# Optimization experiments

Hardware: AMD Instinct MI355X
Metric: run time of the kernel (lower is better)

The kernel has to match this reference:

```python
import jax, jax.numpy as jnp
import numpy as np

B, N, D, L = 8, 2048, 64, 3

def setup_inputs() -> dict:
    key = jax.random.key(0)
    ks = jax.random.split(key, 8)
    x = jax.random.normal(ks[0], (B, N, D), dtype=jnp.float32)
    # binary adjacency with self-loops so every node degree >= 1
    adj = (jax.random.uniform(ks[1], (B, N, N)) < 0.01).astype(jnp.float32)
    adj = jnp.maximum(adj, jnp.eye(N, dtype=jnp.float32)[None])
    # xavier-style params
    U0 = jax.random.normal(ks[2], (D, D), dtype=jnp.float32) * np.sqrt(2.0 / (D + D))
    b0 = jax.random.uniform(ks[3], (D,), dtype=jnp.float32)
    Us = jax.random.normal(ks[4], (L, D, D), dtype=jnp.float32) * np.sqrt(2.0 / (D + D))
    Q = jax.random.normal(ks[5], (D, D), dtype=jnp.float32) * np.sqrt(2.0 / (D + D))
    P = jax.random.normal(ks[6], (1, D), dtype=jnp.float32) * np.sqrt(2.0 / (1 + D))
    return {"x": x, "adj_mat": adj, "U0": U0, "b0": b0, "Us": Us, "Q": Q, "P": P}

def reference(x, adj_mat, U0, b0, Us, Q, P):
    h = x @ U0 + b0  # [B,N,D]
    mask = (adj_mat > 0).astype(h.dtype)          # [B,N,N]
    deg = adj_mat.sum(axis=1)                      # [B,N] (column sums, matches torch sum(axis=1))
    for l in range(Us.shape[0]):
        agg = jnp.einsum('bji,bjd->bid', mask, h)  # masked neighbor sum per node i
        h = jax.nn.relu((agg @ Us[l]) / deg[..., None])
    m = h.sum(axis=1) / h.shape[1]                 # [B,D] mean over nodes
    out = (P @ jax.nn.relu(Q @ m.T)).squeeze()     # [B]
    return out
```

## Files before the change

### kernel.cpp

```cpp
#include <hip/hip_runtime.h>

#define B 8
#define N 2048
#define D 64
#define BN (B*N)
#define CAP 64

__global__ __launch_bounds__(256) void kSLP(
        const float* __restrict__ adj, const float* __restrict__ x,
        const float* __restrict__ U0, const float* __restrict__ b0,
        unsigned short* __restrict__ cols, int* __restrict__ cnt,
        float* __restrict__ h0) {
    __shared__ unsigned sh[64 * 65 + 64];
    const int tid = threadIdx.x;
    const int bid = blockIdx.x;
    if (bid < 256) {
        unsigned (*lmask)[65] = (unsigned(*)[65])sh;
        int b  = bid >> 5, ck = bid & 31;
        int jb = tid >> 5;
        int cp = tid & 31;
        int c0 = cp * 2, c1 = cp * 2 + 1;
        const float* base = adj + (size_t)b * N * N + (size_t)(jb * 256) * N
                            + ck * 64 + cp * 2;
        for (int ws = 0; ws < 8; ++ws) {
            unsigned w0 = 0, w1 = 0;
#pragma unroll 8
            for (int i = 0; i < 32; ++i) {
                float2 v = *(const float2*)(base + (size_t)(ws * 32 + i) * N);
                w0 |= (v.x != 0.f ? 1u : 0u) << i;
                w1 |= (v.y != 0.f ? 1u : 0u) << i;
            }
            lmask[c0][jb * 8 + ws] = w0;
            lmask[c1][jb * 8 + ws] = w1;
        }
        __syncthreads();
        if (tid < 64) {
            int gcol = b * N + ck * 64 + tid;
            unsigned short* cl = cols + (size_t)gcol * CAP;
            int p = 0;
            for (int w = 0; w < 64; ++w) {
                unsigned m = lmask[tid][w];
                int jbase = w * 32;
                while (m) {
                    int t = __builtin_ctz(m);
                    m &= m - 1;
                    if (p < CAP) cl[p] = (unsigned short)(jbase + t);
                    ++p;
                }
            }
            cnt[gcol] = p;
        }
    } else {
        float* Uld = (float*)sh;
        float* bld = (float*)sh + 4096;
#pragma unroll
        for (int q = 0; q < 16; ++q) Uld[tid + q * 256] = U0[tid + q * 256];
        if (tid < D) bld[tid] = b0[tid];
        __syncthreads();
        int wid = tid >> 6, lane = tid & 63;
        int gw = (bid - 256) * 4 + wid;
        for (int rr = 0; rr < 16; ++rr) {
            int r = gw * 16 + rr;
            float xv = x[(size_t)r * D + lane];
            float o0 = bld[lane], o1 = 0.f, o2 = 0.f, o3 = 0.f;
#pragma unroll
            for (int k = 0; k < D; k += 4) {
                o0 = fmaf(__shfl(xv, k),     Uld[(k)     * D + lane], o0);
                o1 = fmaf(__shfl(xv, k + 1), Uld[(k + 1) * D + lane], o1);
                o2 = fmaf(__shfl(xv, k + 2), Uld[(k + 2) * D + lane], o2);
                o3 = fmaf(__shfl(xv, k + 3), Uld[(k + 3) * D + lane], o3);
            }
            h0[(size_t)r * D + lane] = (o0 + o1) + (o2 + o3);
        }
    }
}

__global__ __launch_bounds__(256) void kL(const float* __restrict__ hin,
        const unsigned short* __restrict__ cols, const int* __restrict__ cnt,
        const float* __restrict__ U, float* __restrict__ hout,
        float* __restrict__ pg) {
    __shared__ float Uld[D * D];
    __shared__ float part[4][D];
    const int tid = threadIdx.x;
    const int bid = blockIdx.x;
#pragma unroll
    for (int q = 0; q < 16; ++q) Uld[tid + q * 256] = U[tid + q * 256];
    __syncthreads();
    int wid = tid >> 6, lane = tid & 63;
    int r0 = bid * 8 + wid * 2, r1 = r0 + 1;
    const float* hb = hin + ((size_t)(r0 >> 11) << 11) * D;
    int ca = cnt[r0], cb = cnt[r1];
    int kma = ca < CAP ? ca : CAP, kmb = cb < CAP ? cb : CAP;
    const unsigned short* la = cols + (size_t)r0 * CAP;
    const unsigned short* lb = cols + (size_t)r1 * CAP;
    float acca = 0.f, accb = 0.f;
    int km = kma > kmb ? kma : kmb;
    for (int k = 0; k < km; k += 8) {
        uint4 wa = *(const uint4*)(la + k);
        uint4 wb = *(const uint4*)(lb + k);
        float a0 = hb[(size_t)(wa.x & 0xffff) * D + lane];
        float a1 = hb[(size_t)(wa.x >> 16)    * D + lane];
        float a2 = hb[(size_t)(wa.y & 0xffff) * D + lane];
        float a3 = hb[(size_t)(wa.y >> 16)    * D + lane];
        float a4 = hb[(size_t)(wa.z & 0xffff) * D + lane];
        float a5 = hb[(size_t)(wa.z >> 16)    * D + lane];
        float a6 = hb[(size_t)(wa.w & 0xffff) * D + lane];
        float a7 = hb[(size_t)(wa.w >> 16)    * D + lane];
        float b0_ = hb[(size_t)(wb.x & 0xffff) * D + lane];
        float b1_ = hb[(size_t)(wb.x >> 16)    * D + lane];
        float b2_ = hb[(size_t)(wb.y & 0xffff) * D + lane];
        float b3_ = hb[(size_t)(wb.y >> 16)    * D + lane];
        float b4_ = hb[(size_t)(wb.z & 0xffff) * D + lane];
        float b5_ = hb[(size_t)(wb.z >> 16)    * D + lane];
        float b6_ = hb[(size_t)(wb.w & 0xffff) * D + lane];
        float b7_ = hb[(size_t)(wb.w >> 16)    * D + lane];
        acca += ((k + 0 < kma ? a0 : 0.f) + (k + 1 < kma ? a1 : 0.f))
              + ((k + 2 < kma ? a2 : 0.f) + (k + 3 < kma ? a3 : 0.f))
              + ((k + 4 < kma ? a4 : 0.f) + (k + 5 < kma ? a5 : 0.f))
              + ((k + 6 < kma ? a6 : 0.f) + (k + 7 < kma ? a7 : 0.f));
        accb += ((k + 0 < kmb ? b0_ : 0.f) + (k + 1 < kmb ? b1_ : 0.f))
              + ((k + 2 < kmb ? b2_ : 0.f) + (k + 3 < kmb ? b3_ : 0.f))
              + ((k + 4 < kmb ? b4_ : 0.f) + (k + 5 < kmb ? b5_ : 0.f))
              + ((k + 6 < kmb ? b6_ : 0.f) + (k + 7 < kmb ? b7_ : 0.f));
    }
    float oa0 = 0.f, oa1 = 0.f, oa2 = 0.f, oa3 = 0.f;
    float ob0 = 0.f, ob1 = 0.f, ob2 = 0.f, ob3 = 0.f;
#pragma unroll
    for (int d = 0; d < D; d += 4) {
        oa0 = fmaf(__shfl(acca, d),     Uld[(d)     * D + lane], oa0);
        ob0 = fmaf(__shfl(accb, d),     Uld[(d)     * D + lane], ob0);
        oa1 = fmaf(__shfl(acca, d + 1), Uld[(d + 1) * D + lane], oa1);
        ob1 = fmaf(__shfl(accb, d + 1), Uld[(d + 1) * D + lane], ob1);
        oa2 = fmaf(__shfl(acca, d + 2), Uld[(d + 2) * D + lane], oa2);
        ob2 = fmaf(__shfl(accb, d + 2), Uld[(d + 2) * D + lane], ob2);
        oa3 = fmaf(__shfl(acca, d + 3), Uld[(d + 3) * D + lane], oa3);
        ob3 = fmaf(__shfl(accb, d + 3), Uld[(d + 3) * D + lane], ob3);
    }
    float outa = fmaxf(((oa0 + oa1) + (oa2 + oa3)) / (float)ca, 0.f);
    float outb = fmaxf(((ob0 + ob1) + (ob2 + ob3)) / (float)cb, 0.f);
    hout[(size_t)r0 * D + lane] = outa;
    hout[(size_t)r1 * D + lane] = outb;
    if (pg != nullptr) {
        part[wid][lane] = outa + outb;
        __syncthreads();
        if (wid == 0)
            pg[(size_t)bid * D + lane] =
                part[0][lane] + part[1][lane] + part[2][lane] + part[3][lane];
    }
}

__global__ __launch_bounds__(512) void kHead(const float* __restrict__ pg,
        const float* __restrict__ Q, const float* __restrict__ P,
        float* __restrict__ out) {
    int wid = threadIdx.x >> 6, lane = threadIdx.x & 63;
    float md = 0.f;
#pragma unroll 8
    for (int k = 0; k < 256; ++k) md += pg[(size_t)(wid * 256 + k) * D + lane];
    md *= (1.0f / N);
    float t = 0.f;
#pragma unroll 8
    for (int k = 0; k < D; ++k) t = fmaf(Q[lane * D + k], __shfl(md, k), t);
    t = fmaxf(t, 0.f);
    float v = t * P[lane];
    for (int off = 32; off; off >>= 1) v += __shfl_down(v, off);
    if (lane == 0) out[wid] = v;
}

extern "C" void kernel_launch(void* const* d_in, const int* in_sizes, int n_in,
                              void* d_out, int out_size, void* d_ws, size_t ws_size,
                              hipStream_t stream) {
    const float* x   = (const float*)d_in[0];
    const float* adj = (const float*)d_in[1];
    const float* U0  = (const float*)d_in[2];
    const float* b0  = (const float*)d_in[3];
    const float* Us  = (const float*)d_in[4];
    const float* Q   = (const float*)d_in[5];
    const float* P   = (const float*)d_in[6];
    float* out = (float*)d_out;

    char* ws = (char*)d_ws;
    size_t off = 0;
    float* h0 = (float*)(ws + off); off += (size_t)BN * D * sizeof(float);
    float* h1 = (float*)(ws + off); off += (size_t)BN * D * sizeof(float);
    unsigned short* cols = (unsigned short*)(ws + off);
    off += (size_t)CAP * BN * sizeof(unsigned short);
    int* cnt = (int*)(ws + off); off += (size_t)BN * sizeof(int);
    float* pg = (float*)(ws + off); off += (size_t)2048 * D * sizeof(float);

    kSLP<<<512, 256, 0, stream>>>(adj, x, U0, b0, cols, cnt, h0);
    kL<<<2048, 256, 0, stream>>>(h0, cols, cnt, Us + 0 * D * D, h1, nullptr);
    kL<<<2048, 256, 0, stream>>>(h1, cols, cnt, Us + 1 * D * D, h0, nullptr);
    kL<<<2048, 256, 0, stream>>>(h0, cols, cnt, Us + 2 * D * D, h1, pg);
    kHead<<<1, 512, 0, stream>>>(pg, Q, P, out);
}
```

Before: 109.2 us.

## Widen adjacency scan to 1024-thread blocks with float4 loads, prefetch neighbor indices

The adjacency-to-list scan now uses 1024-thread blocks where each thread reads a 32-row strip of four columns with float4 loads, replacing the eight sequential strips per thread. The aim is more memory requests in flight for the dominant 128 MB adjacency read. The projection half is remapped to fit the larger block. The layer kernel software-prefetches the next group of neighbor indices and masks them to 11 bits, since the prefetch may read past a node's list.

```diff
diff --git a/kernel.cpp b/kernel.cpp
--- a/kernel.cpp
+++ b/kernel.cpp
@@ -6,7 +6,7 @@
 #define BN (B*N)
 #define CAP 64
 
-__global__ __launch_bounds__(256) void kSLP(
+__global__ __launch_bounds__(1024, 8) void kScanProj(
         const float* __restrict__ adj, const float* __restrict__ x,
         const float* __restrict__ U0, const float* __restrict__ b0,
         unsigned short* __restrict__ cols, int* __restrict__ cnt,
@@ -17,22 +17,23 @@
     if (bid < 256) {
         unsigned (*lmask)[65] = (unsigned(*)[65])sh;
         int b  = bid >> 5, ck = bid & 31;
-        int jb = tid >> 5;
-        int cp = tid & 31;
-        int c0 = cp * 2, c1 = cp * 2 + 1;
-        const float* base = adj + (size_t)b * N * N + (size_t)(jb * 256) * N
-                            + ck * 64 + cp * 2;
-        for (int ws = 0; ws < 8; ++ws) {
-            unsigned w0 = 0, w1 = 0;
+        int cq = tid & 15;
+        int js = tid >> 4;
+        const float* base = adj + (size_t)b * N * N + (size_t)(js * 32) * N
+                            + ck * 64 + cq * 4;
+        unsigned w0 = 0, w1 = 0, w2 = 0, w3 = 0;
 #pragma unroll 8
-            for (int i = 0; i < 32; ++i) {
-                float2 v = *(const float2*)(base + (size_t)(ws * 32 + i) * N);
-                w0 |= (v.x != 0.f ? 1u : 0u) << i;
-                w1 |= (v.y != 0.f ? 1u : 0u) << i;
-            }
-            lmask[c0][jb * 8 + ws] = w0;
-            lmask[c1][jb * 8 + ws] = w1;
+        for (int i = 0; i < 32; ++i) {
+            float4 v = *(const float4*)(base + (size_t)i * N);
+            w0 |= (v.x != 0.f ? 1u : 0u) << i;
+            w1 |= (v.y != 0.f ? 1u : 0u) << i;
+            w2 |= (v.z != 0.f ? 1u : 0u) << i;
+            w3 |= (v.w != 0.f ? 1u : 0u) << i;
         }
+        lmask[cq * 4 + 0][js] = w0;
+        lmask[cq * 4 + 1][js] = w1;
+        lmask[cq * 4 + 2][js] = w2;
+        lmask[cq * 4 + 3][js] = w3;
         __syncthreads();
         if (tid < 64) {
             int gcol = b * N + ck * 64 + tid;
@@ -52,15 +53,16 @@
         }
     } else {
         float* Uld = (float*)sh;
-        float* bld = (float*)sh + 4096;
-#pragma unroll
-        for (int q = 0; q < 16; ++q) Uld[tid + q * 256] = U0[tid + q * 256];
+        float* bld = (float*)(sh + 4096);
+#pragma unroll
+        for (int q = 0; q < 4; ++q) Uld[tid + q * 1024] = U0[tid + q * 1024];
         if (tid < D) bld[tid] = b0[tid];
         __syncthreads();
         int wid = tid >> 6, lane = tid & 63;
-        int gw = (bid - 256) * 4 + wid;
-        for (int rr = 0; rr < 16; ++rr) {
-            int r = gw * 16 + rr;
+        int gw = (bid - 256) * 16 + wid;
+#pragma unroll
+        for (int rr = 0; rr < 4; ++rr) {
+            int r = gw * 4 + rr;
             float xv = x[(size_t)r * D + lane];
             float o0 = bld[lane], o1 = 0.f, o2 = 0.f, o3 = 0.f;
 #pragma unroll
@@ -95,25 +97,27 @@
     const unsigned short* lb = cols + (size_t)r1 * CAP;
     float acca = 0.f, accb = 0.f;
     int km = kma > kmb ? kma : kmb;
+    uint4 wa = *(const uint4*)(la);
+    uint4 wb = *(const uint4*)(lb);
     for (int k = 0; k < km; k += 8) {
-        uint4 wa = *(const uint4*)(la + k);
-        uint4 wb = *(const uint4*)(lb + k);
-        float a0 = hb[(size_t)(wa.x & 0xffff) * D + lane];
-        float a1 = hb[(size_t)(wa.x >> 16)    * D + lane];
-        float a2 = hb[(size_t)(wa.y & 0xffff) * D + lane];
-        float a3 = hb[(size_t)(wa.y >> 16)    * D + lane];
-        float a4 = hb[(size_t)(wa.z & 0xffff) * D + lane];
-        float a5 = hb[(size_t)(wa.z >> 16)    * D + lane];
-        float a6 = hb[(size_t)(wa.w & 0xffff) * D + lane];
-        float a7 = hb[(size_t)(wa.w >> 16)    * D + lane];
-        float b0_ = hb[(size_t)(wb.x & 0xffff) * D + lane];
-        float b1_ = hb[(size_t)(wb.x >> 16)    * D + lane];
-        float b2_ = hb[(size_t)(wb.y & 0xffff) * D + lane];
-        float b3_ = hb[(size_t)(wb.y >> 16)    * D + lane];
-        float b4_ = hb[(size_t)(wb.z & 0xffff) * D + lane];
-        float b5_ = hb[(size_t)(wb.z >> 16)    * D + lane];
-        float b6_ = hb[(size_t)(wb.w & 0xffff) * D + lane];
-        float b7_ = hb[(size_t)(wb.w >> 16)    * D + lane];
+        uint4 na = *(const uint4*)(la + k + 8);
+        uint4 nb = *(const uint4*)(lb + k + 8);
+        float a0 = hb[(size_t)(wa.x & 0x7ff)         * D + lane];
+        float a1 = hb[(size_t)((wa.x >> 16) & 0x7ff) * D + lane];
+        float a2 = hb[(size_t)(wa.y & 0x7ff)         * D + lane];
+        float a3 = hb[(size_t)((wa.y >> 16) & 0x7ff) * D + lane];
+        float a4 = hb[(size_t)(wa.z & 0x7ff)         * D + lane];
+        float a5 = hb[(size_t)((wa.z >> 16) & 0x7ff) * D + lane];
+        float a6 = hb[(size_t)(wa.w & 0x7ff)         * D + lane];
+        float a7 = hb[(size_t)((wa.w >> 16) & 0x7ff) * D + lane];
+        float b0_ = hb[(size_t)(wb.x & 0x7ff)         * D + lane];
+        float b1_ = hb[(size_t)((wb.x >> 16) & 0x7ff) * D + lane];
+        float b2_ = hb[(size_t)(wb.y & 0x7ff)         * D + lane];
+        float b3_ = hb[(size_t)((wb.y >> 16) & 0x7ff) * D + lane];
+        float b4_ = hb[(size_t)(wb.z & 0x7ff)         * D + lane];
+        float b5_ = hb[(size_t)((wb.z >> 16) & 0x7ff) * D + lane];
+        float b6_ = hb[(size_t)(wb.w & 0x7ff)         * D + lane];
+        float b7_ = hb[(size_t)((wb.w >> 16) & 0x7ff) * D + lane];
         acca += ((k + 0 < kma ? a0 : 0.f) + (k + 1 < kma ? a1 : 0.f))
               + ((k + 2 < kma ? a2 : 0.f) + (k + 3 < kma ? a3 : 0.f))
               + ((k + 4 < kma ? a4 : 0.f) + (k + 5 < kma ? a5 : 0.f))
@@ -122,6 +126,7 @@
               + ((k + 2 < kmb ? b2_ : 0.f) + (k + 3 < kmb ? b3_ : 0.f))
               + ((k + 4 < kmb ? b4_ : 0.f) + (k + 5 < kmb ? b5_ : 0.f))
               + ((k + 6 < kmb ? b6_ : 0.f) + (k + 7 < kmb ? b7_ : 0.f));
+        wa = na; wb = nb;
     }
     float oa0 = 0.f, oa1 = 0.f, oa2 = 0.f, oa3 = 0.f;
     float ob0 = 0.f, ob1 = 0.f, ob2 = 0.f, ob3 = 0.f;
@@ -187,7 +192,7 @@
     int* cnt = (int*)(ws + off); off += (size_t)BN * sizeof(int);
     float* pg = (float*)(ws + off); off += (size_t)2048 * D * sizeof(float);
 
-    kSLP<<<512, 256, 0, stream>>>(adj, x, U0, b0, cols, cnt, h0);
+    kScanProj<<<512, 1024, 0, stream>>>(adj, x, U0, b0, cols, cnt, h0);
     kL<<<2048, 256, 0, stream>>>(h0, cols, cnt, Us + 0 * D * D, h1, nullptr);
     kL<<<2048, 256, 0, stream>>>(h1, cols, cnt, Us + 1 * D * D, h0, nullptr);
     kL<<<2048, 256, 0, stream>>>(h0, cols, cnt, Us + 2 * D * D, h1, pg);
```

Result: slower. 139.8 us (+28.0%).

## Widen adjacency scan loads and process four rows per wavefront in layers

Applied to the files above, without the earlier changes.

The adjacency scan now uses 512 blocks, each covering 32 columns. Every thread issues sixteen float4 loads in a batch before building its bitmasks, which is meant to raise memory-level parallelism on the dominant 128 MB read. The layer kernel gives each wavefront four rows instead of two and prefetches the next chunk of column indices, with indices masked to 11 bits. This halves the grid size, and the partial-sum buffer and the head reduction loop shrink to match. The cost is more register pressure from the 16-entry float4 arrays and from the extra accumulators.

```diff
diff --git a/kernel.cpp b/kernel.cpp
--- a/kernel.cpp
+++ b/kernel.cpp
@@ -6,36 +6,53 @@
 #define BN (B*N)
 #define CAP 64
 
-__global__ __launch_bounds__(256) void kSLP(
+__global__ __launch_bounds__(256) void kScanProj(
         const float* __restrict__ adj, const float* __restrict__ x,
         const float* __restrict__ U0, const float* __restrict__ b0,
         unsigned short* __restrict__ cols, int* __restrict__ cnt,
         float* __restrict__ h0) {
-    __shared__ unsigned sh[64 * 65 + 64];
+    __shared__ unsigned sh[4160];
     const int tid = threadIdx.x;
     const int bid = blockIdx.x;
-    if (bid < 256) {
+    if (bid < 512) {
         unsigned (*lmask)[65] = (unsigned(*)[65])sh;
-        int b  = bid >> 5, ck = bid & 31;
-        int jb = tid >> 5;
-        int cp = tid & 31;
-        int c0 = cp * 2, c1 = cp * 2 + 1;
-        const float* base = adj + (size_t)b * N * N + (size_t)(jb * 256) * N
-                            + ck * 64 + cp * 2;
-        for (int ws = 0; ws < 8; ++ws) {
-            unsigned w0 = 0, w1 = 0;
-#pragma unroll 8
-            for (int i = 0; i < 32; ++i) {
-                float2 v = *(const float2*)(base + (size_t)(ws * 32 + i) * N);
-                w0 |= (v.x != 0.f ? 1u : 0u) << i;
-                w1 |= (v.y != 0.f ? 1u : 0u) << i;
-            }
-            lmask[c0][jb * 8 + ws] = w0;
-            lmask[c1][jb * 8 + ws] = w1;
+        int b  = bid >> 6, ck = bid & 63;
+        int cq = tid & 7;
+        int js = tid >> 3;
+        const float* base = adj + (size_t)b * N * N + (size_t)(js * 64) * N
+                            + ck * 32 + cq * 4;
+#pragma unroll
+        for (int w = 0; w < 2; ++w) {
+            unsigned m0 = 0, m1 = 0, m2 = 0, m3 = 0;
+            float4 v[16];
+#pragma unroll
+            for (int i = 0; i < 16; ++i)
+                v[i] = *(const float4*)(base + (size_t)(w * 32 + i) * N);
+#pragma unroll
+            for (int i = 0; i < 16; ++i) {
+                m0 |= (v[i].x != 0.f ? 1u : 0u) << i;
+                m1 |= (v[i].y != 0.f ? 1u : 0u) << i;
+                m2 |= (v[i].z != 0.f ? 1u : 0u) << i;
+                m3 |= (v[i].w != 0.f ? 1u : 0u) << i;
+            }
+#pragma unroll
+            for (int i = 0; i < 16; ++i)
+                v[i] = *(const float4*)(base + (size_t)(w * 32 + 16 + i) * N);
+#pragma unroll
+            for (int i = 0; i < 16; ++i) {
+                m0 |= (v[i].x != 0.f ? 1u : 0u) << (16 + i);
+                m1 |= (v[i].y != 0.f ? 1u : 0u) << (16 + i);
+                m2 |= (v[i].z != 0.f ? 1u : 0u) << (16 + i);
+                m3 |= (v[i].w != 0.f ? 1u : 0u) << (16 + i);
+            }
+            lmask[cq * 4 + 0][js * 2 + w] = m0;
+            lmask[cq * 4 + 1][js * 2 + w] = m1;
+            lmask[cq * 4 + 2][js * 2 + w] = m2;
+            lmask[cq * 4 + 3][js * 2 + w] = m3;
         }
         __syncthreads();
-        if (tid < 64) {
-            int gcol = b * N + ck * 64 + tid;
+        if (tid < 32) {
+            int gcol = b * N + ck * 32 + tid;
             unsigned short* cl = cols + (size_t)gcol * CAP;
             int p = 0;
             for (int w = 0; w < 64; ++w) {
@@ -52,13 +69,13 @@
         }
     } else {
         float* Uld = (float*)sh;
-        float* bld = (float*)sh + 4096;
+        float* bld = (float*)(sh + 4096);
 #pragma unroll
         for (int q = 0; q < 16; ++q) Uld[tid + q * 256] = U0[tid + q * 256];
         if (tid < D) bld[tid] = b0[tid];
         __syncthreads();
         int wid = tid >> 6, lane = tid & 63;
-        int gw = (bid - 256) * 4 + wid;
+        int gw = (bid - 512) * 4 + wid;
         for (int rr = 0; rr < 16; ++rr) {
             int r = gw * 16 + rr;
             float xv = x[(size_t)r * D + lane];
@@ -87,61 +104,63 @@
     for (int q = 0; q < 16; ++q) Uld[tid + q * 256] = U[tid + q * 256];
     __syncthreads();
     int wid = tid >> 6, lane = tid & 63;
-    int r0 = bid * 8 + wid * 2, r1 = r0 + 1;
-    const float* hb = hin + ((size_t)(r0 >> 11) << 11) * D;
-    int ca = cnt[r0], cb = cnt[r1];
-    int kma = ca < CAP ? ca : CAP, kmb = cb < CAP ? cb : CAP;
-    const unsigned short* la = cols + (size_t)r0 * CAP;
-    const unsigned short* lb = cols + (size_t)r1 * CAP;
-    float acca = 0.f, accb = 0.f;
-    int km = kma > kmb ? kma : kmb;
+    int rbase = bid * 16 + wid * 4;
+    const float* hb = hin + ((size_t)(rbase >> 11) << 11) * D;
+    int c[4], kmx[4];
+    const unsigned short* cl[4];
+#pragma unroll
+    for (int q = 0; q < 4; ++q) {
+        int r = rbase + q;
+        c[q] = cnt[r];
+        kmx[q] = c[q] < CAP ? c[q] : CAP;
+        cl[q] = cols + (size_t)r * CAP;
+    }
+    int km01 = kmx[0] > kmx[1] ? kmx[0] : kmx[1];
+    int km23 = kmx[2] > kmx[3] ? kmx[2] : kmx[3];
+    int km = km01 > km23 ? km01 : km23;
+    float acc[4] = {0.f, 0.f, 0.f, 0.f};
+    uint4 w4[4];
+#pragma unroll
+    for (int q = 0; q < 4; ++q) w4[q] = *(const uint4*)(cl[q]);
     for (int k = 0; k < km; k += 8) {
-        uint4 wa = *(const uint4*)(la + k);
-        uint4 wb = *(const uint4*)(lb + k);
-        float a0 = hb[(size_t)(wa.x & 0xffff) * D + lane];
-        float a1 = hb[(size_t)(wa.x >> 16)    * D + lane];
-        float a2 = hb[(size_t)(wa.y & 0xffff) * D + lane];
-        float a3 = hb[(size_t)(wa.y >> 16)    * D + lane];
-        float a4 = hb[(size_t)(wa.z & 0xffff) * D + lane];
-        float a5 = hb[(size_t)(wa.z >> 16)    * D + lane];
-        float a6 = hb[(size_t)(wa.w & 0xffff) * D + lane];
-        float a7 = hb[(size_t)(wa.w >> 16)    * D + lane];
-        float b0_ = hb[(size_t)(wb.x & 0xffff) * D + lane];
-        float b1_ = hb[(size_t)(wb.x >> 16)    * D + lane];
-        float b2_ = hb[(size_t)(wb.y & 0xffff) * D + lane];
-        float b3_ = hb[(size_t)(wb.y >> 16)    * D + lane];
-        float b4_ = hb[(size_t)(wb.z & 0xffff) * D + lane];
-        float b5_ = hb[(size_t)(wb.z >> 16)    * D + lane];
-        float b6_ = hb[(size_t)(wb.w & 0xffff) * D + lane];
-        float b7_ = hb[(size_t)(wb.w >> 16)    * D + lane];
-        acca += ((k + 0 < kma ? a0 : 0.f) + (k + 1 < kma ? a1 : 0.f))
-              + ((k + 2 < kma ? a2 : 0.f) + (k + 3 < kma ? a3 : 0.f))
-              + ((k + 4 < kma ? a4 : 0.f) + (k + 5 < kma ? a5 : 0.f))
-              + ((k + 6 < kma ? a6 : 0.f) + (k + 7 < kma ? a7 : 0.f));
-        accb += ((k + 0 < kmb ? b0_ : 0.f) + (k + 1 < kmb ? b1_ : 0.f))
-              + ((k + 2 < kmb ? b2_ : 0.f) + (k + 3 < kmb ? b3_ : 0.f))
-              + ((k + 4 < kmb ? b4_ : 0.f) + (k + 5 < kmb ? b5_ : 0.f))
-              + ((k + 6 < kmb ? b6_ : 0.f) + (k + 7 < kmb ? b7_ : 0.f));
-    }
-    float oa0 = 0.f, oa1 = 0.f, oa2 = 0.f, oa3 = 0.f;
-    float ob0 = 0.f, ob1 = 0.f, ob2 = 0.f, ob3 = 0.f;
-#pragma unroll
-    for (int d = 0; d < D; d += 4) {
-        oa0 = fmaf(__shfl(acca, d),     Uld[(d)     * D + lane], oa0);
-        ob0 = fmaf(__shfl(accb, d),     Uld[(d)     * D + lane], ob0);
-        oa1 = fmaf(__shfl(acca, d + 1), Uld[(d + 1) * D + lane], oa1);
-        ob1 = fmaf(__shfl(accb, d + 1), Uld[(d + 1) * D + lane], ob1);
-        oa2 = fmaf(__shfl(acca, d + 2), Uld[(d + 2) * D + lane], oa2);
-        ob2 = fmaf(__shfl(accb, d + 2), Uld[(d + 2) * D + lane], ob2);
-        oa3 = fmaf(__shfl(acca, d + 3), Uld[(d + 3) * D + lane], oa3);
-        ob3 = fmaf(__shfl(accb, d + 3), Uld[(d + 3) * D + lane], ob3);
-    }
-    float outa = fmaxf(((oa0 + oa1) + (oa2 + oa3)) / (float)ca, 0.f);
-    float outb = fmaxf(((ob0 + ob1) + (ob2 + ob3)) / (float)cb, 0.f);
-    hout[(size_t)r0 * D + lane] = outa;
-    hout[(size_t)r1 * D + lane] = outb;
+        uint4 nx[4];
+#pragma unroll
+        for (int q = 0; q < 4; ++q) nx[q] = *(const uint4*)(cl[q] + k + 8);
+#pragma unroll
+        for (int q = 0; q < 4; ++q) {
+            float a0 = hb[(size_t)(w4[q].x & 0x7ff)         * D + lane];
+            float a1 = hb[(size_t)((w4[q].x >> 16) & 0x7ff) * D + lane];
+            float a2 = hb[(size_t)(w4[q].y & 0x7ff)         * D + lane];
+            float a3 = hb[(size_t)((w4[q].y >> 16) & 0x7ff) * D + lane];
+            float a4 = hb[(size_t)(w4[q].z & 0x7ff)         * D + lane];
+            float a5 = hb[(size_t)((w4[q].z >> 16) & 0x7ff) * D + lane];
+            float a6 = hb[(size_t)(w4[q].w & 0x7ff)         * D + lane];
+            float a7 = hb[(size_t)((w4[q].w >> 16) & 0x7ff) * D + lane];
+            acc[q] += ((k + 0 < kmx[q] ? a0 : 0.f) + (k + 1 < kmx[q] ? a1 : 0.f))
+                    + ((k + 2 < kmx[q] ? a2 : 0.f) + (k + 3 < kmx[q] ? a3 : 0.f))
+                    + ((k + 4 < kmx[q] ? a4 : 0.f) + (k + 5 < kmx[q] ? a5 : 0.f))
+                    + ((k + 6 < kmx[q] ? a6 : 0.f) + (k + 7 < kmx[q] ? a7 : 0.f));
+        }
+#pragma unroll
+        for (int q = 0; q < 4; ++q) w4[q] = nx[q];
+    }
+    float rsum = 0.f;
+#pragma unroll
+    for (int q = 0; q < 4; ++q) {
+        float o0 = 0.f, o1 = 0.f, o2 = 0.f, o3 = 0.f;
+#pragma unroll
+        for (int d = 0; d < D; d += 4) {
+            o0 = fmaf(__shfl(acc[q], d),     Uld[(d)     * D + lane], o0);
+            o1 = fmaf(__shfl(acc[q], d + 1), Uld[(d + 1) * D + lane], o1);
+            o2 = fmaf(__shfl(acc[q], d + 2), Uld[(d + 2) * D + lane], o2);
+            o3 = fmaf(__shfl(acc[q], d + 3), Uld[(d + 3) * D + lane], o3);
+        }
+        float ov = fmaxf(((o0 + o1) + (o2 + o3)) / (float)c[q], 0.f);
+        hout[(size_t)(rbase + q) * D + lane] = ov;
+        rsum += ov;
+    }
     if (pg != nullptr) {
-        part[wid][lane] = outa + outb;
+        part[wid][lane] = rsum;
         __syncthreads();
         if (wid == 0)
             pg[(size_t)bid * D + lane] =
@@ -155,7 +174,7 @@
     int wid = threadIdx.x >> 6, lane = threadIdx.x & 63;
     float md = 0.f;
 #pragma unroll 8
-    for (int k = 0; k < 256; ++k) md += pg[(size_t)(wid * 256 + k) * D + lane];
+    for (int k = 0; k < 128; ++k) md += pg[(size_t)(wid * 128 + k) * D + lane];
     md *= (1.0f / N);
     float t = 0.f;
 #pragma unroll 8
@@ -185,11 +204,11 @@
     unsigned short* cols = (unsigned short*)(ws + off);
     off += (size_t)CAP * BN * sizeof(unsigned short);
     int* cnt = (int*)(ws + off); off += (size_t)BN * sizeof(int);
-    float* pg = (float*)(ws + off); off += (size_t)2048 * D * sizeof(float);
-
-    kSLP<<<512, 256, 0, stream>>>(adj, x, U0, b0, cols, cnt, h0);
-    kL<<<2048, 256, 0, stream>>>(h0, cols, cnt, Us + 0 * D * D, h1, nullptr);
-    kL<<<2048, 256, 0, stream>>>(h1, cols, cnt, Us + 1 * D * D, h0, nullptr);
-    kL<<<2048, 256, 0, stream>>>(h0, cols, cnt, Us + 2 * D * D, h1, pg);
+    float* pg = (float*)(ws + off); off += (size_t)1024 * D * sizeof(float);
+
+    kScanProj<<<768, 256, 0, stream>>>(adj, x, U0, b0, cols, cnt, h0);
+    kL<<<1024, 256, 0, stream>>>(h0, cols, cnt, Us + 0 * D * D, h1, nullptr);
+    kL<<<1024, 256, 0, stream>>>(h1, cols, cnt, Us + 1 * D * D, h0, nullptr);
+    kL<<<1024, 256, 0, stream>>>(h0, cols, cnt, Us + 2 * D * D, h1, pg);
     kHead<<<1, 512, 0, stream>>>(pg, Q, P, out);
 }
```

Measured after the change: 117.9 us. 1.08x slower.
